# Kernel optimization log

Hardware: AMD Instinct MI355X
Metric: run time of the kernel (lower is better)

The kernel has to match this reference:

```python
import jax, jax.numpy as jnp
import numpy as np

B = 64        # number of tasks (sequential steps)
D = 512       # knowledge_representation_dim == understanding_representation_dim
M = 8192      # memory_slots
GAMMA = 0.95  # memory_gamma


def setup_inputs() -> dict:
    key = jax.random.key(0)
    k1, k2, k3, k4 = jax.random.split(key, 4)
    ortho = jax.nn.initializers.orthogonal()
    return {
        "k": jax.random.normal(k1, (B, 1, D), jnp.float32),
        "u": jax.random.normal(k2, (B, 1, D), jnp.float32),
        "memory_knowledge": ortho(k3, (D, M), jnp.float32),
        "memory_understanding": ortho(k4, (D, M), jnp.float32),
        "beta_param": jnp.float32(0.0),
        "memory_gamma": jnp.float32(GAMMA),
    }


def reference(k, u, memory_knowledge, memory_understanding, beta_param, memory_gamma):
    n_slots = memory_knowledge.shape[1]
    slot_ids = jnp.arange(n_slots)
    beta = jax.nn.sigmoid(beta_param)

    def step(carry, xs):
        MK, MU, w_w, w_u, w_lu = carry
        k_task, u_task = xs  # each [1, D]
        # cosine similarity of the task key against every memory column: [1, M]
        sim = (k_task @ MK) / (
            jnp.linalg.norm(k_task, axis=-1, keepdims=True)
            * jnp.linalg.norm(MK, axis=0, keepdims=True)
        )
        w_r = jax.nn.softmax(sim, axis=-1)[0]  # [M]
        # zero out the least-used slot (argmin of usage weights)
        keep = (slot_ids != jnp.argmin(w_u))[None, :]  # [1, M]
        MK = jnp.where(keep, MK, 0.0)
        MU = jnp.where(keep, MU, 0.0)
        # usage / write / least-used weight updates
        w_u = memory_gamma * w_u + w_r + w_w
        w_w = beta * jnp.mean(w_r) + (1.0 - beta) * w_lu  # [M] via broadcast of scalar mean
        w_lu = (slot_ids == jnp.argmin(w_u)).astype(MK.dtype)  # one-hot least-used
        # rank-1 write of understanding, then read refined understanding, then write knowledge
        MU = MU + u_task[0][:, None] * w_w[None, :]  # [D, M]
        u_ref = w_r @ MK.T  # [D] -- read uses MK after zeroing, before its write
        MK = MK + k_task[0][:, None] * w_w[None, :]  # [D, M]
        return (MK, MU, w_w, w_u, w_lu), u_ref

    zeros = jnp.zeros((n_slots,), memory_knowledge.dtype)
    init = (memory_knowledge, memory_understanding, zeros, zeros, zeros)
    _, u_refined = jax.lax.scan(step, init, (k, u))
    return u_refined[:, None, :]  # [B, 1, D]
```

## Files before the change

### kernel.cpp

```cpp
#include <hip/hip_runtime.h>
#include <math.h>

#define BB 64
#define DD 512
#define MM 8192
#define K2T 512
#define K2C 16

typedef unsigned long long u64;

template<int CTRL>
__device__ __forceinline__ float dpp_addf(float x) {
    int y = __builtin_amdgcn_update_dpp(0, __float_as_int(x), CTRL, 0xF, 0xF, true);
    return x + __int_as_float(y);
}
__device__ __forceinline__ float wave_sum64(float x) {
    x = dpp_addf<0x111>(x); x = dpp_addf<0x112>(x); x = dpp_addf<0x114>(x); x = dpp_addf<0x118>(x);
    x = dpp_addf<0x142>(x); x = dpp_addf<0x143>(x);
    return __int_as_float(__builtin_amdgcn_readlane(__float_as_int(x), 63));
}
template<int CTRL>
__device__ __forceinline__ u64 dpp_min_step(u64 k) {
    unsigned lo = (unsigned)k, hi = (unsigned)(k >> 32);
    unsigned nlo = (unsigned)__builtin_amdgcn_update_dpp((int)0xFFFFFFFFu, (int)lo, CTRL, 0xF, 0xF, false);
    unsigned nhi = (unsigned)__builtin_amdgcn_update_dpp((int)0xFFFFFFFFu, (int)hi, CTRL, 0xF, 0xF, false);
    u64 nk = (((u64)nhi) << 32) | (u64)nlo;
    return nk < k ? nk : k;
}
__device__ __forceinline__ u64 wave_min64_lane63(u64 k) {
    k = dpp_min_step<0x111>(k); k = dpp_min_step<0x112>(k); k = dpp_min_step<0x114>(k);
    k = dpp_min_step<0x118>(k); k = dpp_min_step<0x142>(k); k = dpp_min_step<0x143>(k);
    return k;
}
__device__ __forceinline__ u64 wave_min8(u64 k) {
    k = dpp_min_step<0x111>(k); k = dpp_min_step<0x112>(k); k = dpp_min_step<0x114>(k);
    unsigned lo = (unsigned)__builtin_amdgcn_readlane((int)(unsigned)k, 7);
    unsigned hi = (unsigned)__builtin_amdgcn_readlane((int)(unsigned)(k >> 32), 7);
    return (((u64)hi) << 32) | (u64)lo;
}
__device__ __forceinline__ float readlane_f(float v, int l) {
    return __int_as_float(__builtin_amdgcn_readlane(__float_as_int(v), l));
}

struct K0Smem {
    float Ks[BB][129];
    float Gs[BB][BB];
};
struct K1Smem {
    float Ks[64 * 65];
    float Ms[64 * 65];
    float sq[4 * 64];
};
#define KA_SMEM ((sizeof(K0Smem) > sizeof(K1Smem)) ? sizeof(K0Smem) : sizeof(K1Smem))

__global__ __launch_bounds__(256) void ka_gram_s0(const float* __restrict__ K, const float* __restrict__ MK0,
                                                  float* __restrict__ G, float* __restrict__ Pfx,
                                                  float* __restrict__ S0p, float* __restrict__ n2p) {
    __shared__ __align__(16) char blob[KA_SMEM];
    const int tid = threadIdx.x;

    if (blockIdx.x == 0) {
        K0Smem* sm = (K0Smem*)blob;
        const int ti = ((tid >> 4) & 15) << 2;
        const int tj = (tid & 15) << 2;
        float acc[4][4];
        #pragma unroll
        for (int i = 0; i < 4; ++i)
            #pragma unroll
            for (int j = 0; j < 4; ++j) acc[i][j] = 0.f;
        for (int d0 = 0; d0 < DD; d0 += 128) {
            #pragma unroll
            for (int i = 0; i < 32; ++i) {
                int e = i * 256 + tid; int r = e >> 7, c = e & 127;
                sm->Ks[r][c] = K[r * DD + d0 + c];
            }
            __syncthreads();
            for (int dl = 0; dl < 128; ++dl) {
                float rv[4], cv[4];
                #pragma unroll
                for (int i = 0; i < 4; ++i) rv[i] = sm->Ks[ti + i][dl];
                #pragma unroll
                for (int j = 0; j < 4; ++j) cv[j] = sm->Ks[tj + j][dl];
                #pragma unroll
                for (int i = 0; i < 4; ++i)
                    #pragma unroll
                    for (int j = 0; j < 4; ++j) acc[i][j] += rv[i] * cv[j];
            }
            __syncthreads();
        }
        #pragma unroll
        for (int i = 0; i < 4; ++i)
            #pragma unroll
            for (int j = 0; j < 4; ++j) {
                G[(ti + i) * BB + tj + j] = acc[i][j];
                sm->Gs[ti + i][tj + j] = acc[i][j];
            }
        __syncthreads();
        const int s = tid & 63, w = tid >> 6;
        for (int rr = 0; rr < 16; ++rr) {
            int row = w * 16 + rr;
            float x = (s < row) ? sm->Gs[row][s] : 0.f;
            #pragma unroll
            for (int o = 1; o < 64; o <<= 1) {
                float y = __shfl_down(x, o);
                if (s + o < 64) x += y;
            }
            Pfx[row * BB + s] = x;
        }
        return;
    }

    K1Smem* sm = (K1Smem*)blob;
    const int b = blockIdx.x - 1;
    const int lane = tid & 63, w = tid >> 6;
    const int jb = (b & 127) * 64;
    const int by = b >> 7;
    const int dbase = by * 256;
    const int t4 = ((w << 2) | (lane >> 4)) << 2;
    const int jq0 = lane & 15;
    float acc[4][4];
    #pragma unroll
    for (int i = 0; i < 4; ++i)
        #pragma unroll
        for (int q = 0; q < 4; ++q) acc[i][q] = 0.f;
    float sqa = 0.f;
    for (int dt = 0; dt < 4; ++dt) {
        int d0 = dbase + dt * 64;
        #pragma unroll
        for (int i = 0; i < 16; ++i) {
            int e = i * 256 + tid; int r = e >> 6, c = e & 63;
            sm->Ks[r * 65 + c] = K[r * DD + d0 + c];
            float m = MK0[(d0 + r) * MM + jb + c];
            sm->Ms[r * 65 + c] = m;
            sqa += m * m;
        }
        __syncthreads();
        #pragma unroll 4
        for (int dl = 0; dl < 64; ++dl) {
            float kv[4], mv[4];
            #pragma unroll
            for (int i = 0; i < 4; ++i) kv[i] = sm->Ks[(t4 + i) * 65 + dl];
            #pragma unroll
            for (int q = 0; q < 4; ++q) mv[q] = sm->Ms[dl * 65 + jq0 + 16 * q];
            #pragma unroll
            for (int i = 0; i < 4; ++i)
                #pragma unroll
                for (int q = 0; q < 4; ++q) acc[i][q] += kv[i] * mv[q];
        }
        __syncthreads();
    }
    #pragma unroll
    for (int i = 0; i < 4; ++i)
        #pragma unroll
        for (int q = 0; q < 4; ++q)
            S0p[by * BB * MM + (t4 + i) * MM + jb + jq0 + 16 * q] = acc[i][q];
    sm->sq[w * 64 + lane] = sqa;
    __syncthreads();
    if (w == 0) n2p[by * MM + jb + lane] =
        sm->sq[lane] + sm->sq[64 + lane] + sm->sq[128 + lane] + sm->sq[192 + lane];
}

__global__ __launch_bounds__(64) void k1b_ecold(const float* __restrict__ S0p,
                                                const float* __restrict__ G,
                                                const float* __restrict__ Pfx,
                                                const float* __restrict__ n2p,
                                                const float* __restrict__ bp,
                                                float* __restrict__ Ecold) {
    __shared__ float Pfx0s[BB], invks[BB], k2s[BB];
    int tid = threadIdx.x;
    int j = blockIdx.x * 64 + tid;
    {
        float g = G[tid * BB + tid];
        k2s[tid] = g;
        invks[tid] = __builtin_amdgcn_rsqf(g);
        Pfx0s[tid] = Pfx[tid * BB + 0];
    }
    const float beta = 1.f / (1.f + expf(-bp[0]));
    const float cuni = beta / (float)MM;
    float n2c = n2p[j] + n2p[MM + j];
    __syncthreads();
    float pa = S0p[j];
    float pb = S0p[BB * MM + j];
    for (int t = 0; t < BB; ++t) {
        float na = 0.f, nb = 0.f;
        if (t + 1 < BB) {
            na = S0p[(t + 1) * MM + j];
            nb = S0p[(BB + t + 1) * MM + j];
        }
        float s0 = pa + pb;
        float d_ = s0 + cuni * Pfx0s[t];
        float cosv = d_ * invks[t] * __builtin_amdgcn_rsqf(n2c);
        float ee = __expf(cosv);
        Ecold[t * MM + j] = ee;
        n2c = n2c + 2.f * cuni * d_ + cuni * cuni * k2s[t];
        pa = na; pb = nb;
    }
}

__global__ __launch_bounds__(256) void ks_rowsum(const float* __restrict__ Ecold, float* __restrict__ Scold) {
    __shared__ float sw[4];
    int t = blockIdx.x, tid = threadIdx.x;
    int lane = tid & 63, wid = tid >> 6;
    float s = 0.f;
    #pragma unroll
    for (int i = 0; i < 32; ++i) s += Ecold[t * MM + i * 256 + tid];
    #pragma unroll
    for (int o = 32; o > 0; o >>= 1) s += __shfl_down(s, o);
    if (lane == 0) sw[wid] = s;
    __syncthreads();
    if (tid == 0) Scold[t] = sw[0] + sw[1] + sw[2] + sw[3];
}

struct ScanSmem {
    u64   red[2][8];
    int   endL[BB];
    float invS_bc;
};
struct K3Smem {
    float Ws[64 * 65];
    float Msub[64 * 65];
};
#define SMEM_BYTES ((sizeof(ScanSmem) > sizeof(K3Smem)) ? sizeof(ScanSmem) : sizeof(K3Smem))

__global__ __launch_bounds__(512) void k23_scan_u1(const float* __restrict__ Ecold,
                                                   const float* __restrict__ G,
                                                   const float* __restrict__ Pfx,
                                                   const float* __restrict__ Scoldg,
                                                   const float* __restrict__ bp,
                                                   const float* __restrict__ gp,
                                                   const float* __restrict__ MK0,
                                                   float* __restrict__ Etab_g,
                                                   float* __restrict__ EcTab_g,
                                                   float* __restrict__ Sg,
                                                   float* __restrict__ invSg,
                                                   int*   __restrict__ endTab_g,
                                                   int*   __restrict__ hcolg,
                                                   float* __restrict__ parts) {
    __shared__ __align__(16) char smem_raw[SMEM_BYTES];
    const int tid = threadIdx.x;

    if (blockIdx.x != 0) {
        K3Smem* sm = (K3Smem*)smem_raw;
        for (int tile = blockIdx.x - 1; tile < 256; tile += 255) {
            const int d0 = (tile & 7) * 64;
            const int by = tile >> 3;
            const bool act = tid < 256;
            const int lane = tid & 63, w = tid >> 6;
            const int t4 = ((w << 2) | (lane >> 4)) << 2;
            const int dq0 = lane & 15;
            float acc[4][4];
            #pragma unroll
            for (int i = 0; i < 4; ++i)
                #pragma unroll
                for (int q = 0; q < 4; ++q) acc[i][q] = 0.f;
            for (int sub = 0; sub < 4; ++sub) {
                int jb = by * 256 + sub * 64;
                if (act) {
                    #pragma unroll
                    for (int i = 0; i < 16; ++i) {
                        int e = i * 256 + tid; int r = e >> 6, c = e & 63;
                        sm->Ws[r * 65 + c] = Ecold[r * MM + jb + c];
                        sm->Msub[r * 65 + c] = MK0[(d0 + r) * MM + jb + c];
                    }
                }
                __syncthreads();
                if (act) {
                    #pragma unroll 4
                    for (int jl = 0; jl < 64; ++jl) {
                        float wv[4], mv[4];
                        #pragma unroll
                        for (int i = 0; i < 4; ++i) wv[i] = sm->Ws[(t4 + i) * 65 + jl];
                        #pragma unroll
                        for (int q = 0; q < 4; ++q) mv[q] = sm->Msub[(dq0 + 16 * q) * 65 + jl];
                        #pragma unroll
                        for (int i = 0; i < 4; ++i)
                            #pragma unroll
                            for (int q = 0; q < 4; ++q) acc[i][q] += wv[i] * mv[q];
                    }
                }
                __syncthreads();
            }
            if (act) {
                #pragma unroll
                for (int i = 0; i < 4; ++i)
                    #pragma unroll
                    for (int q = 0; q < 4; ++q)
                        parts[(by * 64 + t4 + i) * DD + d0 + dq0 + 16 * q] = acc[i][q];
            }
            __syncthreads();
        }
        return;
    }

    ScanSmem* sm = (ScanSmem*)smem_raw;
    const int lane = tid & 63;
    const int wid = tid >> 6;
    const bool w0 = (wid == 0);

    const float beta  = 1.f / (1.f + expf(-bp[0]));
    const float gamma = gp[0];
    const float cuni  = beta / (float)MM;
    const float omb   = 1.f - beta;

    if (tid < BB) sm->endL[tid] = BB;

    const float4* Ec4 = reinterpret_cast<const float4*>(Ecold);

    float wu[K2C], e0[K2C], e1[K2C], e2[K2C];
    #pragma unroll
    for (int c = 0; c < K2C; ++c) wu[c] = 0.f;
    #pragma unroll
    for (int i = 0; i < K2C / 4; ++i) {
        float4 v = Ec4[i * K2T + tid];
        e0[4 * i + 0] = v.x; e0[4 * i + 1] = v.y; e0[4 * i + 2] = v.z; e0[4 * i + 3] = v.w;
        float4 u = Ec4[(MM / 4) + i * K2T + tid];
        e1[4 * i + 0] = u.x; e1[4 * i + 1] = u.y; e1[4 * i + 2] = u.z; e1[4 * i + 3] = u.w;
    }

    float slot_n2 = 0.f, slot_E = 0.f, slot_ec = 0.f, slot_ecpf = 0.f, wu_hot = 0.f;
    int   slot_j = -1;
    bool  slot_act = false;

    float grow_c = 0.f, pfx_c = 0.f, Ssc_c = 0.f;
    if (w0) { grow_c = G[lane]; pfx_c = Pfx[lane]; Ssc_c = Scoldg[0]; }
    __syncthreads();

    auto step = [&](int t, float (&cur)[K2C], float (&ld)[K2C]) {
        int j0; float minval;
        if (t == 0) { j0 = 0; minval = 0.f; }
        else {
            u64 pm = sm->red[t & 1][lane & 7];
            pm = wave_min8(pm);
            j0 = (int)(pm & 0xFFFFFFFFu);
            minval = __uint_as_float((unsigned)(pm >> 32));
        }
        const float cuni_t = (t == 0) ? 0.f : cuni;

        float latev = 0.f;
        if (w0 && lane == t) latev = Ecold[t * MM + j0];
        if (w0 && t + 1 < BB) {
            int js = (lane == t) ? j0 : slot_j;
            if (slot_act || lane == t) slot_ecpf = Ecold[(t + 1) * MM + js];
        }
        float grow_n = 0.f, pfx_n = 0.f, Ssc_n = 0.f;
        if (w0 && t + 1 < BB) {
            grow_n = G[(t + 1) * BB + lane];
            pfx_n  = Pfx[(t + 1) * BB + lane];
            Ssc_n  = Scoldg[t + 1];
        }
        __builtin_amdgcn_sched_barrier(0);
        if (t + 2 < BB) {
            #pragma unroll
            for (int i = 0; i < K2C / 4; ++i) {
                float4 v = Ec4[(t + 2) * (MM / 4) + i * K2T + tid];
                ld[4 * i + 0] = v.x; ld[4 * i + 1] = v.y; ld[4 * i + 2] = v.z; ld[4 * i + 3] = v.w;
            }
        }
        __builtin_amdgcn_sched_barrier(0);

        float invS = 0.f, S = 0.f, e_true = 0.f;
        bool fresh = false;
        if (w0) {
            const float k2t  = readlane_f(grow_c, t);
            const float invk = __builtin_amdgcn_rsqf(k2t);

            u64 sup = __ballot(slot_act && (slot_j == j0));
            const bool has_sup = (sup != 0ull);
            const int  ssup = has_sup ? (int)__builtin_ctzll(sup) : 0;

            float myDelta = 0.f;
            if (slot_act) {
                float d_ = cuni * pfx_c;
                if (lane >= 1) d_ += omb * grow_c;
                e_true = __expf(d_ * invk * __builtin_amdgcn_rsqf(slot_n2));
                myDelta = e_true - slot_ec;
                slot_E = e_true;
                slot_n2 = slot_n2 + 2.f * cuni * d_ + cuni * cuni * k2t;
            }

            S = Ssc_c + wave_sum64(myDelta);
            invS = __builtin_amdgcn_rcpf(S);
            sm->invS_bc = invS;

            if (slot_act) {
                float ww = cuni + ((t >= 2 && lane == t - 1) ? omb : 0.f);
                wu_hot = fmaf(gamma, wu_hot, fmaf(e_true, invS, ww));
            }

            float trans_wu = readlane_f(wu_hot, ssup);
            float trans_E  = readlane_f(e_true, ssup);
            if (lane == t) {
                slot_j = j0;
                float ww0 = cuni + ((t >= 1) ? omb : 0.f);
                slot_n2 = ww0 * ww0 * k2t;
                slot_act = true;
                if (has_sup) { wu_hot = trans_wu; slot_E = trans_E; }
                fresh = !has_sup;
            }
            if (has_sup) {
                if (lane == ssup) slot_act = false;
                if (lane == t) sm->endL[ssup] = t;
            }
        }

        asm volatile("s_waitcnt lgkmcnt(0)" ::: "memory");
        __builtin_amdgcn_s_barrier();
        asm volatile("" ::: "memory");
        if (!w0) invS = sm->invS_bc;

        u64 kk[K2C];
        #pragma unroll
        for (int i = 0; i < 4; ++i) {
            #pragma unroll
            for (int q = 0; q < 4; ++q) {
                int c = i * 4 + q;
                float wun = fmaf(gamma, wu[c], fmaf(cur[c], invS, cuni_t));
                wu[c] = wun;
                int j = i * 2048 + (tid << 2) + q;
                kk[c] = (((u64)__float_as_uint(wun)) << 32) | (unsigned)j;
            }
        }
        #pragma unroll
        for (int s = 8; s >= 1; s >>= 1)
            #pragma unroll
            for (int c = 0; c < s; ++c)
                kk[c] = kk[c + s] < kk[c] ? kk[c + s] : kk[c];
        u64 key = kk[0];

        if (((j0 >> 2) & (K2T - 1)) == tid) {
            int cj = ((j0 >> 11) << 2) | (j0 & 3);
            #pragma unroll
            for (int c = 0; c < K2C; ++c) if (c == cj) wu[c] = __builtin_inff();
        }

        if (w0) {
            u64 skey = (slot_act && !fresh)
                     ? ((((u64)__float_as_uint(wu_hot)) << 32) | (unsigned)slot_j) : ~0ull;
            key = skey < key ? skey : key;
        }
        key = wave_min64_lane63(key);
        if (lane == 63) sm->red[(t + 1) & 1][wid] = key;

        if (w0) {
            if (lane == t) slot_ec = latev;
            if (fresh) {
                slot_E  = latev;
                wu_hot  = fmaf(gamma, minval, fmaf(latev, invS, cuni_t));
            }
            Etab_g[t * BB + lane]  = slot_E;
            EcTab_g[t * BB + lane] = slot_ec;
            if (lane == 0) { invSg[t] = invS; Sg[t] = S; }
            if (slot_act) slot_ec = slot_ecpf;
            grow_c = grow_n; pfx_c = pfx_n; Ssc_c = Ssc_n;
        }

        asm volatile("s_waitcnt lgkmcnt(0)" ::: "memory");
        __builtin_amdgcn_s_barrier();
        asm volatile("" ::: "memory");
    };

    #pragma unroll 1
    for (int th = 0; th < 63; th += 3) {
        step(th + 0, e0, e2);
        step(th + 1, e1, e0);
        step(th + 2, e2, e1);
    }
    step(63, e0, e2);

    if (tid < BB) endTab_g[tid] = sm->endL[tid];
    if (w0) hcolg[lane] = slot_j;
}

__global__ __launch_bounds__(512) void k3b_gather(const float* __restrict__ MK0, const int* __restrict__ hcolg,
                                                  float* __restrict__ MKhot) {
    int i = blockIdx.x, d = threadIdx.x;
    int h = hcolg[i];
    MKhot[i * DD + d] = MK0[d * MM + h];
}

__global__ __launch_bounds__(512) void k4_final(const float* __restrict__ parts,
                                                const float* __restrict__ K,
                                                const float* __restrict__ Etab,
                                                const float* __restrict__ EcTab,
                                                const int*   __restrict__ endTab,
                                                const float* __restrict__ Sg,
                                                const float* __restrict__ invSg,
                                                const float* __restrict__ MKhot,
                                                const float* __restrict__ bp,
                                                float* __restrict__ out) {
    __shared__ float Arow[BB];
    __shared__ float Drow[BB];
    int t = blockIdx.x, d = threadIdx.x;
    if (d < BB) {
        const float beta = 1.f / (1.f + expf(-bp[0]));
        const float cuni = beta / (float)MM;
        const float omb  = 1.f - beta;
        int s = d;
        float Ev = Etab[t * BB + s];
        int endv = endTab[s];
        bool act = (s <= t) && (t < endv);
        float S = Sg[t], invS = invSg[t];
        float ev = act ? Ev : 0.f;
        float x = ev;
        #pragma unroll
        for (int o = 1; o < 64; o <<= 1) {
            float y = __shfl_down(x, o);
            if (s + o < 64) x += y;
        }
        float suf = x - ev;
        float arow = 0.f;
        if (s < t) {
            float Qe = S - suf;
            arow = cuni * Qe;
            if (s >= 1 && act) arow += omb * Ev;
            arow *= invS;
        }
        Arow[s] = arow;
        Drow[s] = act ? (-invS * EcTab[t * BB + s]) : 0.f;
    }
    __syncthreads();
    float isv = invSg[t];
    float s1 = 0.f;
    #pragma unroll
    for (int p = 0; p < 32; ++p) s1 += parts[(p * 64 + t) * DD + d];
    float s2 = 0.f;
    for (int i = 0; i < BB; ++i) s2 += Drow[i] * MKhot[i * DD + d];
    float s3 = 0.f;
    for (int i = 0; i < BB; ++i) s3 += Arow[i] * K[i * DD + d];
    out[t * DD + d] = isv * s1 + s2 + s3;
}

extern "C" void kernel_launch(void* const* d_in, const int* in_sizes, int n_in,
                              void* d_out, int out_size, void* d_ws, size_t ws_size,
                              hipStream_t stream) {
    const float* K   = (const float*)d_in[0];
    const float* MK0 = (const float*)d_in[2];
    const float* bp  = (const float*)d_in[4];
    const float* gp  = (const float*)d_in[5];

    float* ws    = (float*)d_ws;
    float* G     = ws;
    float* Pfx   = G + 4096;
    float* S0p   = Pfx + 4096;
    float* n2p   = S0p + 1048576;
    float* Ecold = n2p + 16384;
    float* Scold = Ecold + 524288;
    float* Etab  = Scold + 64;
    float* EcTab = Etab + 4096;
    float* Sarr  = EcTab + 4096;
    float* invS  = Sarr + 64;
    float* MKhot = invS + 64;
    float* parts = MKhot + 32768;
    int*   hcol  = (int*)(parts + 1048576);
    int*   endT  = hcol + 64;
    float* out   = (float*)d_out;

    ka_gram_s0  <<<257, 256, 0, stream>>>(K, MK0, G, Pfx, S0p, n2p);
    k1b_ecold   <<<128, 64, 0, stream>>>(S0p, G, Pfx, n2p, bp, Ecold);
    ks_rowsum   <<<64, 256, 0, stream>>>(Ecold, Scold);
    k23_scan_u1 <<<256, 512, 0, stream>>>(Ecold, G, Pfx, Scold, bp, gp, MK0,
                                          Etab, EcTab, Sarr, invS, endT, hcol, parts);
    k3b_gather  <<<64, 512, 0, stream>>>(MK0, hcol, MKhot);
    k4_final    <<<64, 512, 0, stream>>>(parts, K, Etab, EcTab, endT, Sarr, invS, MKhot, bp, out);
}
```

Before: 225.1 us.

## Precompute next-step normalizer in scan, buffer tables in LDS, one tile per block

```diff
diff --git a/kernel.cpp b/kernel.cpp
--- a/kernel.cpp
+++ b/kernel.cpp
@@ -18,6 +18,9 @@
     x = dpp_addf<0x111>(x); x = dpp_addf<0x112>(x); x = dpp_addf<0x114>(x); x = dpp_addf<0x118>(x);
     x = dpp_addf<0x142>(x); x = dpp_addf<0x143>(x);
     return __int_as_float(__builtin_amdgcn_readlane(__float_as_int(x), 63));
+}
+__device__ __forceinline__ float readlane_f(float v, int l) {
+    return __int_as_float(__builtin_amdgcn_readlane(__float_as_int(v), l));
 }
 template<int CTRL>
 __device__ __forceinline__ u64 dpp_min_step(u64 k) {
@@ -37,9 +40,6 @@
     unsigned lo = (unsigned)__builtin_amdgcn_readlane((int)(unsigned)k, 7);
     unsigned hi = (unsigned)__builtin_amdgcn_readlane((int)(unsigned)(k >> 32), 7);
     return (((u64)hi) << 32) | (u64)lo;
-}
-__device__ __forceinline__ float readlane_f(float v, int l) {
-    return __int_as_float(__builtin_amdgcn_readlane(__float_as_int(v), l));
 }
 
 struct K0Smem {
@@ -213,8 +213,12 @@
 
 struct ScanSmem {
     u64   red[2][8];
+    float EtabL[BB * BB];
+    float EcTabL[BB * BB];
+    float invSL[BB];
+    float SL[BB];
     int   endL[BB];
-    float invS_bc;
+    float invS_bc[2];
 };
 struct K3Smem {
     float Ws[64 * 65];
@@ -241,53 +245,51 @@
 
     if (blockIdx.x != 0) {
         K3Smem* sm = (K3Smem*)smem_raw;
-        for (int tile = blockIdx.x - 1; tile < 256; tile += 255) {
-            const int d0 = (tile & 7) * 64;
-            const int by = tile >> 3;
-            const bool act = tid < 256;
-            const int lane = tid & 63, w = tid >> 6;
-            const int t4 = ((w << 2) | (lane >> 4)) << 2;
-            const int dq0 = lane & 15;
-            float acc[4][4];
+        const int tile = blockIdx.x - 1;
+        const int d0 = (tile & 7) * 64;
+        const int by = tile >> 3;
+        const bool act = tid < 256;
+        const int lane = tid & 63, w = tid >> 6;
+        const int t4 = ((w << 2) | (lane >> 4)) << 2;
+        const int dq0 = lane & 15;
+        float acc[4][4];
+        #pragma unroll
+        for (int i = 0; i < 4; ++i)
+            #pragma unroll
+            for (int q = 0; q < 4; ++q) acc[i][q] = 0.f;
+        for (int sub = 0; sub < 4; ++sub) {
+            int jb = by * 256 + sub * 64;
+            if (act) {
+                #pragma unroll
+                for (int i = 0; i < 16; ++i) {
+                    int e = i * 256 + tid; int r = e >> 6, c = e & 63;
+                    sm->Ws[r * 65 + c] = Ecold[r * MM + jb + c];
+                    sm->Msub[r * 65 + c] = MK0[(d0 + r) * MM + jb + c];
+                }
+            }
+            __syncthreads();
+            if (act) {
+                #pragma unroll 4
+                for (int jl = 0; jl < 64; ++jl) {
+                    float wv[4], mv[4];
+                    #pragma unroll
+                    for (int i = 0; i < 4; ++i) wv[i] = sm->Ws[(t4 + i) * 65 + jl];
+                    #pragma unroll
+                    for (int q = 0; q < 4; ++q) mv[q] = sm->Msub[(dq0 + 16 * q) * 65 + jl];
+                    #pragma unroll
+                    for (int i = 0; i < 4; ++i)
+                        #pragma unroll
+                        for (int q = 0; q < 4; ++q) acc[i][q] += wv[i] * mv[q];
+                }
+            }
+            __syncthreads();
+        }
+        if (act) {
             #pragma unroll
             for (int i = 0; i < 4; ++i)
                 #pragma unroll
-                for (int q = 0; q < 4; ++q) acc[i][q] = 0.f;
-            for (int sub = 0; sub < 4; ++sub) {
-                int jb = by * 256 + sub * 64;
-                if (act) {
-                    #pragma unroll
-                    for (int i = 0; i < 16; ++i) {
-                        int e = i * 256 + tid; int r = e >> 6, c = e & 63;
-                        sm->Ws[r * 65 + c] = Ecold[r * MM + jb + c];
-                        sm->Msub[r * 65 + c] = MK0[(d0 + r) * MM + jb + c];
-                    }
-                }
-                __syncthreads();
-                if (act) {
-                    #pragma unroll 4
-                    for (int jl = 0; jl < 64; ++jl) {
-                        float wv[4], mv[4];
-                        #pragma unroll
-                        for (int i = 0; i < 4; ++i) wv[i] = sm->Ws[(t4 + i) * 65 + jl];
-                        #pragma unroll
-                        for (int q = 0; q < 4; ++q) mv[q] = sm->Msub[(dq0 + 16 * q) * 65 + jl];
-                        #pragma unroll
-                        for (int i = 0; i < 4; ++i)
-                            #pragma unroll
-                            for (int q = 0; q < 4; ++q) acc[i][q] += wv[i] * mv[q];
-                    }
-                }
-                __syncthreads();
-            }
-            if (act) {
-                #pragma unroll
-                for (int i = 0; i < 4; ++i)
-                    #pragma unroll
-                    for (int q = 0; q < 4; ++q)
-                        parts[(by * 64 + t4 + i) * DD + d0 + dq0 + 16 * q] = acc[i][q];
-            }
-            __syncthreads();
+                for (int q = 0; q < 4; ++q)
+                    parts[(by * 64 + t4 + i) * DD + d0 + dq0 + 16 * q] = acc[i][q];
         }
         return;
     }
@@ -317,15 +319,29 @@
         e1[4 * i + 0] = u.x; e1[4 * i + 1] = u.y; e1[4 * i + 2] = u.z; e1[4 * i + 3] = u.w;
     }
 
-    float slot_n2 = 0.f, slot_E = 0.f, slot_ec = 0.f, slot_ecpf = 0.f, wu_hot = 0.f;
+    float slot_n2 = 0.f, slot_ec = 0.f, wu_hot = 0.f, e_true_c = 0.f;
     int   slot_j = -1;
     bool  slot_act = false;
-
-    float grow_c = 0.f, pfx_c = 0.f, Ssc_c = 0.f;
-    if (w0) { grow_c = G[lane]; pfx_c = Pfx[lane]; Ssc_c = Scoldg[0]; }
+    float k2_cur = 0.f, S_reg = 0.f, invS_reg = 0.f;
+
+    if (w0) {
+        float g0 = G[lane];
+        k2_cur = readlane_f(g0, 0);
+        S_reg = Scoldg[0];
+        invS_reg = __builtin_amdgcn_rcpf(S_reg);
+        if (lane == 0) sm->invS_bc[0] = invS_reg;
+    }
     __syncthreads();
 
     auto step = [&](int t, float (&cur)[K2C], float (&ld)[K2C]) {
+        float grow_n = 0.f, pfx_n = 0.f, Ssc_n = 0.f, ecpf0 = 0.f;
+        if (w0 && t + 1 < BB) {
+            if (slot_act) ecpf0 = Ecold[(t + 1) * MM + slot_j];
+            grow_n = G[(t + 1) * BB + lane];
+            pfx_n  = Pfx[(t + 1) * BB + lane];
+            Ssc_n  = Scoldg[t + 1];
+        }
+
         int j0; float minval;
         if (t == 0) { j0 = 0; minval = 0.f; }
         else {
@@ -335,18 +351,12 @@
             minval = __uint_as_float((unsigned)(pm >> 32));
         }
         const float cuni_t = (t == 0) ? 0.f : cuni;
-
-        float latev = 0.f;
-        if (w0 && lane == t) latev = Ecold[t * MM + j0];
-        if (w0 && t + 1 < BB) {
-            int js = (lane == t) ? j0 : slot_j;
-            if (slot_act || lane == t) slot_ecpf = Ecold[(t + 1) * MM + js];
-        }
-        float grow_n = 0.f, pfx_n = 0.f, Ssc_n = 0.f;
-        if (w0 && t + 1 < BB) {
-            grow_n = G[(t + 1) * BB + lane];
-            pfx_n  = Pfx[(t + 1) * BB + lane];
-            Ssc_n  = Scoldg[t + 1];
+        float invS = w0 ? invS_reg : sm->invS_bc[t & 1];
+
+        float latev = 0.f, ecpf_t = 0.f;
+        if (w0 && lane == t) {
+            latev = Ecold[t * MM + j0];
+            if (t + 1 < BB) ecpf_t = Ecold[(t + 1) * MM + j0];
         }
         __builtin_amdgcn_sched_barrier(0);
         if (t + 2 < BB) {
@@ -358,57 +368,64 @@
         }
         __builtin_amdgcn_sched_barrier(0);
 
-        float invS = 0.f, S = 0.f, e_true = 0.f;
         bool fresh = false;
         if (w0) {
-            const float k2t  = readlane_f(grow_c, t);
-            const float invk = __builtin_amdgcn_rsqf(k2t);
-
             u64 sup = __ballot(slot_act && (slot_j == j0));
             const bool has_sup = (sup != 0ull);
             const int  ssup = has_sup ? (int)__builtin_ctzll(sup) : 0;
 
-            float myDelta = 0.f;
-            if (slot_act) {
-                float d_ = cuni * pfx_c;
-                if (lane >= 1) d_ += omb * grow_c;
-                e_true = __expf(d_ * invk * __builtin_amdgcn_rsqf(slot_n2));
-                myDelta = e_true - slot_ec;
-                slot_E = e_true;
-                slot_n2 = slot_n2 + 2.f * cuni * d_ + cuni * cuni * k2t;
-            }
-
-            S = Ssc_c + wave_sum64(myDelta);
-            invS = __builtin_amdgcn_rcpf(S);
-            sm->invS_bc = invS;
-
             if (slot_act) {
                 float ww = cuni + ((t >= 2 && lane == t - 1) ? omb : 0.f);
-                wu_hot = fmaf(gamma, wu_hot, fmaf(e_true, invS, ww));
-            }
-
+                wu_hot = fmaf(gamma, wu_hot, fmaf(e_true_c, invS, ww));
+            }
             float trans_wu = readlane_f(wu_hot, ssup);
-            float trans_E  = readlane_f(e_true, ssup);
+            float trans_E  = readlane_f(e_true_c, ssup);
+
             if (lane == t) {
                 slot_j = j0;
                 float ww0 = cuni + ((t >= 1) ? omb : 0.f);
-                slot_n2 = ww0 * ww0 * k2t;
+                slot_n2 = ww0 * ww0 * k2_cur;
                 slot_act = true;
-                if (has_sup) { wu_hot = trans_wu; slot_E = trans_E; }
+                if (has_sup) wu_hot = trans_wu;
                 fresh = !has_sup;
             }
             if (has_sup) {
                 if (lane == ssup) slot_act = false;
                 if (lane == t) sm->endL[ssup] = t;
             }
-        }
-
-        asm volatile("s_waitcnt lgkmcnt(0)" ::: "memory");
-        __builtin_amdgcn_s_barrier();
-        asm volatile("" ::: "memory");
-        if (!w0) invS = sm->invS_bc;
-
-        u64 kk[K2C];
+
+            float etl = e_true_c, ecl = slot_ec;
+            if (lane == t) { ecl = latev; etl = has_sup ? trans_E : latev; }
+            sm->EtabL[t * BB + lane]  = etl;
+            sm->EcTabL[t * BB + lane] = ecl;
+            if (lane == 0) { sm->invSL[t] = invS; sm->SL[t] = S_reg; }
+
+            if (fresh) wu_hot = fmaf(gamma, minval, fmaf(latev, invS, cuni_t));
+
+            if (t + 1 < BB) {
+                float d_ = cuni * pfx_n;
+                if (lane >= 1) d_ += omb * grow_n;
+                float k2n   = readlane_f(grow_n, t + 1);
+                float invkn = __builtin_amdgcn_rsqf(k2n);
+                float ecpf  = (lane == t) ? ecpf_t : ecpf0;
+                float myDelta = 0.f;
+                float e_n = 0.f;
+                if (slot_act) {
+                    e_n = __expf(d_ * invkn * __builtin_amdgcn_rsqf(slot_n2));
+                    myDelta = e_n - ecpf;
+                    slot_n2 = slot_n2 + 2.f * cuni * d_ + cuni * cuni * k2n;
+                }
+                float S_next = Ssc_n + wave_sum64(myDelta);
+                float invS_next = __builtin_amdgcn_rcpf(S_next);
+                if (lane == 0) sm->invS_bc[(t + 1) & 1] = invS_next;
+                if (slot_act) slot_ec = ecpf;
+                e_true_c = e_n;
+                k2_cur = k2n;
+                S_reg = S_next; invS_reg = invS_next;
+            }
+        }
+
+        float vmin = 0.f; int jmin = 0;
         #pragma unroll
         for (int i = 0; i < 4; ++i) {
             #pragma unroll
@@ -417,15 +434,11 @@
                 float wun = fmaf(gamma, wu[c], fmaf(cur[c], invS, cuni_t));
                 wu[c] = wun;
                 int j = i * 2048 + (tid << 2) + q;
-                kk[c] = (((u64)__float_as_uint(wun)) << 32) | (unsigned)j;
-            }
-        }
-        #pragma unroll
-        for (int s = 8; s >= 1; s >>= 1)
-            #pragma unroll
-            for (int c = 0; c < s; ++c)
-                kk[c] = kk[c + s] < kk[c] ? kk[c + s] : kk[c];
-        u64 key = kk[0];
+                if (c == 0) { vmin = wun; jmin = j; }
+                else if (wun < vmin) { vmin = wun; jmin = j; }
+            }
+        }
+        u64 key = (((u64)__float_as_uint(vmin)) << 32) | (unsigned)jmin;
 
         if (((j0 >> 2) & (K2T - 1)) == tid) {
             int cj = ((j0 >> 11) << 2) | (j0 & 3);
@@ -440,19 +453,6 @@
         }
         key = wave_min64_lane63(key);
         if (lane == 63) sm->red[(t + 1) & 1][wid] = key;
-
-        if (w0) {
-            if (lane == t) slot_ec = latev;
-            if (fresh) {
-                slot_E  = latev;
-                wu_hot  = fmaf(gamma, minval, fmaf(latev, invS, cuni_t));
-            }
-            Etab_g[t * BB + lane]  = slot_E;
-            EcTab_g[t * BB + lane] = slot_ec;
-            if (lane == 0) { invSg[t] = invS; Sg[t] = S; }
-            if (slot_act) slot_ec = slot_ecpf;
-            grow_c = grow_n; pfx_c = pfx_n; Ssc_c = Ssc_n;
-        }
 
         asm volatile("s_waitcnt lgkmcnt(0)" ::: "memory");
         __builtin_amdgcn_s_barrier();
@@ -467,7 +467,15 @@
     }
     step(63, e0, e2);
 
-    if (tid < BB) endTab_g[tid] = sm->endL[tid];
+    for (int i = tid; i < BB * BB; i += K2T) {
+        Etab_g[i]  = sm->EtabL[i];
+        EcTab_g[i] = sm->EcTabL[i];
+    }
+    if (tid < BB) {
+        Sg[tid] = sm->SL[tid];
+        invSg[tid] = sm->invSL[tid];
+        endTab_g[tid] = sm->endL[tid];
+    }
     if (w0) hcolg[lane] = slot_j;
 }
 
@@ -558,7 +566,7 @@
     ka_gram_s0  <<<257, 256, 0, stream>>>(K, MK0, G, Pfx, S0p, n2p);
     k1b_ecold   <<<128, 64, 0, stream>>>(S0p, G, Pfx, n2p, bp, Ecold);
     ks_rowsum   <<<64, 256, 0, stream>>>(Ecold, Scold);
-    k23_scan_u1 <<<256, 512, 0, stream>>>(Ecold, G, Pfx, Scold, bp, gp, MK0,
+    k23_scan_u1 <<<257, 512, 0, stream>>>(Ecold, G, Pfx, Scold, bp, gp, MK0,
                                           Etab, EcTab, Sarr, invS, endT, hcol, parts);
     k3b_gather  <<<64, 512, 0, stream>>>(MK0, hcol, MKhot);
     k4_final    <<<64, 512, 0, stream>>>(parts, K, Etab, EcTab, endT, Sarr, invS, MKhot, bp, out);
```

Result: faster. 214.6 us (-4.7%).
